# Kernel tuning notes

Measured on AMD Instinct MI355X. Metric: run time of the kernel, lower is better.

Reference implementation:

```python
import jax, jax.numpy as jnp
import numpy as np

N = 20000      # nodes
E = 320000     # edges (every node has >=1 incoming edge)
IN = 512       # input feature dim
HID = 128      # per-head hidden dim
H = 8          # heads
C = 64         # classes (final layer hidden dim)
SLOPE = 0.01   # torch F.leaky_relu default negative_slope


def _gat_head(x, src, dst, W, b, al, alb, ar, arb):
    # x: [N, D_in]; W: [D_in, D_h]; al/ar: [D_h]; alb/arb: scalar
    ft = x @ W + b                       # [N, D_h]
    a1 = ft @ al + alb                   # [N] dst-side logit
    a2 = ft @ ar + arb                   # [N] src-side logit
    s = jax.nn.leaky_relu(a1[dst] + a2[src], SLOPE)   # [E]
    smax = jax.ops.segment_max(s, dst, num_segments=N)
    e = jnp.exp(s - smax[dst])
    denom = jax.ops.segment_sum(e, dst, num_segments=N)
    w = e / denom[dst]                   # segment softmax over incoming edges
    accum = jax.ops.segment_sum(w[:, None] * ft[src], dst, num_segments=N)
    return jax.nn.elu(accum)             # GATFinalize (no residual)


def setup_inputs() -> dict:
    key = jax.random.key(0)
    ks = jax.random.split(key, 16)

    def lin(k, i, o):
        return (jax.random.normal(k, (i, o), jnp.float32) / np.sqrt(i))

    features = jax.random.normal(ks[0], (N, IN), jnp.float32)
    src = jax.random.randint(ks[1], (E,), 0, N, jnp.int32)
    dst = jnp.concatenate([
        jnp.arange(N, dtype=jnp.int32),
        jax.random.randint(ks[2], (E - N,), 0, N, jnp.int32),
    ])

    # layer 0: H heads, in_dim -> HID
    W0 = jax.random.normal(ks[3], (H, IN, HID), jnp.float32) / np.sqrt(IN)
    b0 = jnp.zeros((H, HID), jnp.float32)
    al0 = jax.random.normal(ks[4], (H, HID), jnp.float32) / np.sqrt(HID)
    alb0 = jnp.zeros((H,), jnp.float32)
    ar0 = jax.random.normal(ks[5], (H, HID), jnp.float32) / np.sqrt(HID)
    arb0 = jnp.zeros((H,), jnp.float32)

    # layer 1: H heads, H*HID -> HID
    W1 = jax.random.normal(ks[6], (H, H * HID, HID), jnp.float32) / np.sqrt(H * HID)
    b1 = jnp.zeros((H, HID), jnp.float32)
    al1 = jax.random.normal(ks[7], (H, HID), jnp.float32) / np.sqrt(HID)
    alb1 = jnp.zeros((H,), jnp.float32)
    ar1 = jax.random.normal(ks[8], (H, HID), jnp.float32) / np.sqrt(HID)
    arb1 = jnp.zeros((H,), jnp.float32)

    # final: single head, H*HID -> C
    Wf = lin(ks[9], H * HID, C)
    bf = jnp.zeros((C,), jnp.float32)
    alf = jax.random.normal(ks[10], (C,), jnp.float32) / np.sqrt(C)
    albf = jnp.zeros((), jnp.float32)
    arf = jax.random.normal(ks[11], (C,), jnp.float32) / np.sqrt(C)
    arbf = jnp.zeros((), jnp.float32)

    return dict(features=features, src=src, dst=dst,
                W0=W0, b0=b0, al0=al0, alb0=alb0, ar0=ar0, arb0=arb0,
                W1=W1, b1=b1, al1=al1, alb1=alb1, ar1=ar1, arb1=arb1,
                Wf=Wf, bf=bf, alf=alf, albf=albf, arf=arf, arbf=arbf)


def reference(features, src, dst,
              W0, b0, al0, alb0, ar0, arb0,
              W1, b1, al1, alb1, ar1, arb1,
              Wf, bf, alf, albf, arf, arbf):
    x = features
    # layer 0: concat heads -> [N, H*HID]
    x = jnp.concatenate([
        _gat_head(x, src, dst, W0[h], b0[h], al0[h], alb0[h], ar0[h], arb0[h])
        for h in range(H)], axis=1)
    # layer 1
    x = jnp.concatenate([
        _gat_head(x, src, dst, W1[h], b1[h], al1[h], alb1[h], ar1[h], arb1[h])
        for h in range(H)], axis=1)
    # final single-head output layer -> [N, C]
    return _gat_head(x, src, dst, Wf, bf, alf, albf, arf, arbf)
```

## Files before the change

kernel.cpp:

```cpp
#include <hip/hip_runtime.h>
#include <math.h>

#define N_NODES 20000
#define N_EDGES 320000
#define D_IN    512
#define D_HID   128
#define N_HEADS 8
#define N_CLS   64

typedef __bf16 bf16x8 __attribute__((ext_vector_type(8)));
typedef float  f32x4  __attribute__((ext_vector_type(4)));

__device__ __forceinline__ float leaky(float x) { return fmaxf(x, 0.01f * x); }

__device__ __forceinline__ unsigned short f2bf(float f) {
    unsigned u = __float_as_uint(f);
    return (unsigned short)((u + 0x7FFFu + ((u >> 16) & 1u)) >> 16);
}
__device__ __forceinline__ float bflo(unsigned v) { return __uint_as_float(v << 16); }
__device__ __forceinline__ float bfhi(unsigned v) { return __uint_as_float(v & 0xffff0000u); }

__device__ __forceinline__ void gl_lds16(const void* g, void* l) {
    __builtin_amdgcn_global_load_lds((const __attribute__((address_space(1))) void*)g,
                                     (__attribute__((address_space(3))) void*)l, 16, 0, 0);
}

__global__ void k_zero(int* __restrict__ p, int n) {
    int i = blockIdx.x * blockDim.x + threadIdx.x;
    if (i < n) p[i] = 0;
}

__global__ void k_count(const int* __restrict__ dst, int* __restrict__ counts, int e) {
    int i = blockIdx.x * blockDim.x + threadIdx.x;
    if (i < e) atomicAdd(&counts[dst[i]], 1);
}

__global__ void k_scan(const int* __restrict__ counts, int* __restrict__ indptr,
                       int* __restrict__ cursor, int n) {
    __shared__ int sdata[1024];
    __shared__ int srun;
    int t = threadIdx.x;
    if (t == 0) srun = 0;
    __syncthreads();
    for (int base = 0; base < n; base += 1024) {
        int idx = base + t;
        int v = (idx < n) ? counts[idx] : 0;
        sdata[t] = v;
        __syncthreads();
        for (int off = 1; off < 1024; off <<= 1) {
            int x = (t >= off) ? sdata[t - off] : 0;
            __syncthreads();
            sdata[t] += x;
            __syncthreads();
        }
        int incl = sdata[t];
        int run = srun;
        if (idx < n) {
            indptr[idx] = run + incl - v;
            cursor[idx] = run + incl - v;
        }
        __syncthreads();
        if (t == 1023) srun = run + incl;
        __syncthreads();
    }
    if (t == 0) indptr[n] = srun;
}

__global__ void k_scatter(const int* __restrict__ src, const int* __restrict__ dst,
                          int* __restrict__ cursor, int* __restrict__ csr_src, int e) {
    int i = blockIdx.x * blockDim.x + threadIdx.x;
    if (i < e) {
        int pos = atomicAdd(&cursor[dst[i]], 1);
        csr_src[pos] = src[i];
    }
}

__global__ void k_cvtA(const float* __restrict__ in, unsigned short* __restrict__ out, int n4) {
    int i = blockIdx.x * blockDim.x + threadIdx.x;
    if (i < n4) {
        float4 v = ((const float4*)in)[i];
        unsigned long long pk =
            (unsigned long long)f2bf(v.x) | ((unsigned long long)f2bf(v.y) << 16) |
            ((unsigned long long)f2bf(v.z) << 32) | ((unsigned long long)f2bf(v.w) << 48);
        *(unsigned long long*)(out + (size_t)i * 4) = pk;
    }
}

__global__ void k_cvtW(const float* __restrict__ W, unsigned short* __restrict__ Wt,
                       int K, int Nf) {
    __shared__ float t[64][65];
    int k0 = blockIdx.x * 64, n0 = blockIdx.y * 64, h = blockIdx.z;
    const float* Wh = W + (size_t)h * K * Nf;
    unsigned short* Wth = Wt + (size_t)h * K * Nf;
    int tx = threadIdx.x & 63, ty = threadIdx.x >> 6;
#pragma unroll
    for (int i = 0; i < 16; ++i) {
        int k = ty + i * 4;
        t[k][tx] = Wh[(size_t)(k0 + k) * Nf + n0 + tx];
    }
    __syncthreads();
#pragma unroll
    for (int i = 0; i < 16; ++i) {
        int n = ty + i * 4;
        Wth[(size_t)(n0 + n) * K + k0 + tx] = f2bf(t[tx][n]);
    }
}

__global__ __launch_bounds__(256) void k_gemm_fused(
    const unsigned short* __restrict__ A, const unsigned short* __restrict__ Bt,
    const float* __restrict__ bias, const float* __restrict__ al,
    const float* __restrict__ alb, const float* __restrict__ ar,
    const float* __restrict__ arb, unsigned short* __restrict__ C,
    float* __restrict__ a1, float* __restrict__ a2, int M, int K)
{
    constexpr int BM = 128, BK = 64, BNP = 256;
    __shared__ unsigned short As[BM * BK];
    __shared__ unsigned short Bs[BNP * BK];

    const int tid  = threadIdx.x;
    const int lane = tid & 63;
    const int wid  = tid >> 6;
    const int wm   = wid >> 1;
    const int wn   = wid & 1;
    const int m0   = blockIdx.x * BM;
    const int h0   = blockIdx.z * 2;
    const int h    = h0 + wn;

    const unsigned short* Bth = Bt + (size_t)h0 * 128 * K;
    const int rsub = lane & 15;
    const int rhi  = lane >> 4;
    const int wbase = tid & ~63;

    f32x4 acc[4][8];
#pragma unroll
    for (int i = 0; i < 4; ++i)
#pragma unroll
        for (int j = 0; j < 8; ++j) acc[i][j] = (f32x4){0.f, 0.f, 0.f, 0.f};

    for (int k0 = 0; k0 < K; k0 += BK) {
#pragma unroll
        for (int p = 0; p < 4; ++p) {
            int o    = (p * 256 + tid) * 16;
            int row  = o >> 7;
            int icol = (o & 127) ^ ((row & 7) << 4);
            int grow = m0 + row; if (grow > M - 1) grow = M - 1;
            gl_lds16(A + (size_t)grow * K + k0 + (icol >> 1),
                     (void*)((char*)As + (p * 256 + wbase) * 16));
        }
#pragma unroll
        for (int p = 0; p < 8; ++p) {
            int o    = (p * 256 + tid) * 16;
            int row  = o >> 7;
            int icol = (o & 127) ^ ((row & 7) << 4);
            gl_lds16(Bth + (size_t)row * K + k0 + (icol >> 1),
                     (void*)((char*)Bs + (p * 256 + wbase) * 16));
        }
        __syncthreads();

#pragma unroll
        for (int q = 0; q < 2; ++q) {
            bf16x8 av[4], bv[8];
#pragma unroll
            for (int mi = 0; mi < 4; ++mi) {
                int row  = wm * 64 + mi * 16 + rsub;
                int icol = (q * 64 + rhi * 16) ^ ((row & 7) << 4);
                av[mi] = *(const bf16x8*)((const char*)As + row * 128 + icol);
            }
#pragma unroll
            for (int ni = 0; ni < 8; ++ni) {
                int row  = wn * 128 + ni * 16 + rsub;
                int icol = (q * 64 + rhi * 16) ^ ((row & 7) << 4);
                bv[ni] = *(const bf16x8*)((const char*)Bs + row * 128 + icol);
            }
#pragma unroll
            for (int mi = 0; mi < 4; ++mi)
#pragma unroll
                for (int ni = 0; ni < 8; ++ni)
                    acc[mi][ni] = __builtin_amdgcn_mfma_f32_16x16x32_bf16(
                        av[mi], bv[ni], acc[mi][ni], 0, 0, 0);
        }
        __syncthreads();
    }

#pragma unroll
    for (int ni = 0; ni < 8; ++ni) {
        float bvv = bias[h * 128 + ni * 16 + rsub];
#pragma unroll
        for (int mi = 0; mi < 4; ++mi)
#pragma unroll
            for (int r = 0; r < 4; ++r) acc[mi][ni][r] += bvv;
    }

#pragma unroll
    for (int ni = 0; ni < 8; ++ni) {
        int col = h * 128 + ni * 16 + rsub;
#pragma unroll
        for (int mi = 0; mi < 4; ++mi) {
            int rowb = m0 + wm * 64 + mi * 16 + rhi * 4;
#pragma unroll
            for (int r = 0; r < 4; ++r) {
                int row = rowb + r;
                if (row < M) C[(size_t)row * 1024 + col] = f2bf(acc[mi][ni][r]);
            }
        }
    }

    float alv[8], arv[8];
#pragma unroll
    for (int ni = 0; ni < 8; ++ni) {
        alv[ni] = al[h * 128 + ni * 16 + rsub];
        arv[ni] = ar[h * 128 + ni * 16 + rsub];
    }
    float albv = alb[h], arbv = arb[h];
#pragma unroll
    for (int mi = 0; mi < 4; ++mi) {
#pragma unroll
        for (int r = 0; r < 4; ++r) {
            float s1 = 0.f, s2 = 0.f;
#pragma unroll
            for (int ni = 0; ni < 8; ++ni) {
                s1 += acc[mi][ni][r] * alv[ni];
                s2 += acc[mi][ni][r] * arv[ni];
            }
#pragma unroll
            for (int off = 1; off <= 8; off <<= 1) {
                s1 += __shfl_xor(s1, off);
                s2 += __shfl_xor(s2, off);
            }
            if (rsub == 0) {
                int row = m0 + wm * 64 + mi * 16 + rhi * 4 + r;
                if (row < M) {
                    a1[row * 8 + h] = s1 + albv;
                    a2[row * 8 + h] = s2 + arbv;
                }
            }
        }
    }
}

template<int BN>
__global__ __launch_bounds__(256) void k_gemm_bf16(
    const unsigned short* __restrict__ A, const unsigned short* __restrict__ Bt,
    const float* __restrict__ bias, unsigned short* __restrict__ C,
    int M, int K, int ldc)
{
    constexpr int BM = 128, BK = 64;
    constexpr int WN    = 1;
    constexpr int MFRAG = 2;
    constexpr int NFRAG = 4;

    __shared__ unsigned short As[BM * BK];
    __shared__ unsigned short Bs[BN * BK];

    const int tid  = threadIdx.x;
    const int lane = tid & 63;
    const int wid  = tid >> 6;
    const int wm   = wid / WN;
    const int wn   = wid % WN;
    const int m0   = blockIdx.x * BM;

    const int rsub = lane & 15;
    const int rhi  = lane >> 4;
    const int wbase = tid & ~63;

    f32x4 acc[MFRAG][NFRAG];
#pragma unroll
    for (int i = 0; i < MFRAG; ++i)
#pragma unroll
        for (int j = 0; j < NFRAG; ++j) acc[i][j] = (f32x4){0.f, 0.f, 0.f, 0.f};

    for (int k0 = 0; k0 < K; k0 += BK) {
#pragma unroll
        for (int p = 0; p < 4; ++p) {
            int o    = (p * 256 + tid) * 16;
            int row  = o >> 7;
            int icol = (o & 127) ^ ((row & 7) << 4);
            int grow = m0 + row; if (grow > M - 1) grow = M - 1;
            gl_lds16(A + (size_t)grow * K + k0 + (icol >> 1),
                     (void*)((char*)As + (p * 256 + wbase) * 16));
        }
#pragma unroll
        for (int p = 0; p < BN / 32; ++p) {
            int o    = (p * 256 + tid) * 16;
            int row  = o >> 7;
            int icol = (o & 127) ^ ((row & 7) << 4);
            gl_lds16(Bt + (size_t)row * K + k0 + (icol >> 1),
                     (void*)((char*)Bs + (p * 256 + wbase) * 16));
        }
        __syncthreads();

        bf16x8 av[2][MFRAG], bv[2][NFRAG];
#pragma unroll
        for (int q = 0; q < 2; ++q) {
#pragma unroll
            for (int mi = 0; mi < MFRAG; ++mi) {
                int row  = wm * (MFRAG * 16) + mi * 16 + rsub;
                int icol = (q * 64 + rhi * 16) ^ ((row & 7) << 4);
                av[q][mi] = *(const bf16x8*)((const char*)As + row * 128 + icol);
            }
#pragma unroll
            for (int ni = 0; ni < NFRAG; ++ni) {
                int row  = wn * (NFRAG * 16) + ni * 16 + rsub;
                int icol = (q * 64 + rhi * 16) ^ ((row & 7) << 4);
                bv[q][ni] = *(const bf16x8*)((const char*)Bs + row * 128 + icol);
            }
        }
#pragma unroll
        for (int q = 0; q < 2; ++q)
#pragma unroll
            for (int mi = 0; mi < MFRAG; ++mi)
#pragma unroll
                for (int ni = 0; ni < NFRAG; ++ni)
                    acc[mi][ni] = __builtin_amdgcn_mfma_f32_16x16x32_bf16(
                        av[q][mi], bv[q][ni], acc[mi][ni], 0, 0, 0);
        __syncthreads();
    }

#pragma unroll
    for (int ni = 0; ni < NFRAG; ++ni) {
        int col  = wn * (NFRAG * 16) + ni * 16 + rsub;
        float bvv = bias[col];
#pragma unroll
        for (int mi = 0; mi < MFRAG; ++mi) {
            int rowb = m0 + wm * (MFRAG * 16) + mi * 16 + rhi * 4;
#pragma unroll
            for (int r = 0; r < 4; ++r) {
                int row = rowb + r;
                if (row < M) C[(size_t)row * ldc + col] = f2bf(acc[mi][ni][r] + bvv);
            }
        }
    }
}

__global__ __launch_bounds__(256) void k_alogit(
    const unsigned short* __restrict__ ft, const float* __restrict__ al,
    const float* __restrict__ alb, const float* __restrict__ ar,
    const float* __restrict__ arb, float* __restrict__ a1,
    float* __restrict__ a2, int H_, int Dh)
{
    int n = blockIdx.x * 4 + (threadIdx.x >> 6);
    int lane = threadIdx.x & 63;
    if (n >= N_NODES) return;
    for (int h = 0; h < H_; ++h) {
        size_t base = ((size_t)h * N_NODES + n) * Dh;
        float s1 = 0.f, s2 = 0.f;
        for (int j0 = 2 * lane; j0 < Dh; j0 += 128) {
            unsigned v = *(const unsigned*)(ft + base + j0);
            float lo = bflo(v), hi = bfhi(v);
            float2 A = *(const float2*)(al + h * Dh + j0);
            float2 R = *(const float2*)(ar + h * Dh + j0);
            s1 += lo * A.x + hi * A.y;
            s2 += lo * R.x + hi * R.y;
        }
#pragma unroll
        for (int off = 32; off > 0; off >>= 1) {
            s1 += __shfl_xor(s1, off);
            s2 += __shfl_xor(s2, off);
        }
        if (lane == 0) {
            a1[n * H_ + h] = s1 + alb[h];
            a2[n * H_ + h] = s2 + arb[h];
        }
    }
}

__global__ __launch_bounds__(256) void k_aggregate_ah(
    const unsigned short* __restrict__ ft, const float* __restrict__ a1,
    const float* __restrict__ a2, const int* __restrict__ indptr,
    const int* __restrict__ csr_src, unsigned short* __restrict__ outp)
{
    __shared__ float wtab[2][4][64][8];
    __shared__ int   stab[2][4][64];

    const int wid  = threadIdx.x >> 6;
    const int lane = threadIdx.x & 63;
    int n = blockIdx.x * 4 + wid;
    if (n >= N_NODES) return;
    int start = indptr[n], end = indptr[n + 1];
    unsigned short* op = outp + (size_t)n * 1024;

    if (end <= start) {
        uint4 z = make_uint4(0, 0, 0, 0);
        *(uint4*)(op + lane * 8) = z;
        *(uint4*)(op + 512 + lane * 8) = z;
        return;
    }

    float a1v[8];
    *(float4*)&a1v[0] = *(const float4*)(a1 + n * 8);
    *(float4*)&a1v[4] = *(const float4*)(a1 + n * 8 + 4);

    float m[8], sv0[8];
    int sidx0 = 0;
#pragma unroll
    for (int h = 0; h < 8; ++h) { m[h] = -INFINITY; sv0[h] = -INFINITY; }
    {
        int e = start + lane;
        if (e < end) {
            sidx0 = csr_src[e];
            float4 x0 = *(const float4*)(a2 + (size_t)sidx0 * 8);
            float4 x1 = *(const float4*)(a2 + (size_t)sidx0 * 8 + 4);
            sv0[0] = leaky(a1v[0] + x0.x); sv0[1] = leaky(a1v[1] + x0.y);
            sv0[2] = leaky(a1v[2] + x0.z); sv0[3] = leaky(a1v[3] + x0.w);
            sv0[4] = leaky(a1v[4] + x1.x); sv0[5] = leaky(a1v[5] + x1.y);
            sv0[6] = leaky(a1v[6] + x1.z); sv0[7] = leaky(a1v[7] + x1.w);
#pragma unroll
            for (int h = 0; h < 8; ++h) m[h] = sv0[h];
        }
        for (int e2 = start + 64 + lane; e2 < end; e2 += 64) {
            int s = csr_src[e2];
            float4 x0 = *(const float4*)(a2 + (size_t)s * 8);
            float4 x1 = *(const float4*)(a2 + (size_t)s * 8 + 4);
            m[0] = fmaxf(m[0], leaky(a1v[0] + x0.x)); m[1] = fmaxf(m[1], leaky(a1v[1] + x0.y));
            m[2] = fmaxf(m[2], leaky(a1v[2] + x0.z)); m[3] = fmaxf(m[3], leaky(a1v[3] + x0.w));
            m[4] = fmaxf(m[4], leaky(a1v[4] + x1.x)); m[5] = fmaxf(m[5], leaky(a1v[5] + x1.y));
            m[6] = fmaxf(m[6], leaky(a1v[6] + x1.z)); m[7] = fmaxf(m[7], leaky(a1v[7] + x1.w));
        }
#pragma unroll
        for (int h = 0; h < 8; ++h)
#pragma unroll
            for (int off = 32; off > 0; off >>= 1)
                m[h] = fmaxf(m[h], __shfl_xor(m[h], off));
    }

    float denom[8];
    float acc[16];
#pragma unroll
    for (int h = 0; h < 8; ++h) denom[h] = 0.f;
#pragma unroll
    for (int i = 0; i < 16; ++i) acc[i] = 0.f;

    int pb = 0;
    for (int base = start; base < end; base += 64, pb ^= 1) {
        int e = base + lane;
        int cnt = min(64, end - base);
        float w[8];
        int sidx = 0;
        if (base == start) {
            sidx = sidx0;
            if (e < end) {
#pragma unroll
                for (int h = 0; h < 8; ++h) w[h] = expf(sv0[h] - m[h]);
            } else {
#pragma unroll
                for (int h = 0; h < 8; ++h) w[h] = 0.f;
            }
        } else if (e < end) {
            sidx = csr_src[e];
            float4 x0 = *(const float4*)(a2 + (size_t)sidx * 8);
            float4 x1 = *(const float4*)(a2 + (size_t)sidx * 8 + 4);
            w[0] = expf(leaky(a1v[0] + x0.x) - m[0]); w[1] = expf(leaky(a1v[1] + x0.y) - m[1]);
            w[2] = expf(leaky(a1v[2] + x0.z) - m[2]); w[3] = expf(leaky(a1v[3] + x0.w) - m[3]);
            w[4] = expf(leaky(a1v[4] + x1.x) - m[4]); w[5] = expf(leaky(a1v[5] + x1.y) - m[5]);
            w[6] = expf(leaky(a1v[6] + x1.z) - m[6]); w[7] = expf(leaky(a1v[7] + x1.w) - m[7]);
        } else {
#pragma unroll
            for (int h = 0; h < 8; ++h) w[h] = 0.f;
        }
#pragma unroll
        for (int h = 0; h < 8; ++h) denom[h] += w[h];

        *(float4*)&wtab[pb][wid][lane][0] = *(float4*)&w[0];
        *(float4*)&wtab[pb][wid][lane][4] = *(float4*)&w[4];
        stab[pb][wid][lane] = sidx;
        asm volatile("s_waitcnt lgkmcnt(0)" ::: "memory");

        const float* wrow = &wtab[pb][wid][0][0];
        const int*   srow = &stab[pb][wid][0];
        const int myh = lane >> 4;
        for (int j = 0; j < cnt; j += 2) {
            int j1ok = (j + 1 < cnt);
            int j1 = j1ok ? j + 1 : j;
            int s0 = srow[j];
            int s1 = srow[j1];
            float w00 = wrow[j * 8 + myh];
            float w01 = wrow[j * 8 + 4 + myh];
            float w10 = j1ok ? wrow[j1 * 8 + myh] : 0.f;
            float w11 = j1ok ? wrow[j1 * 8 + 4 + myh] : 0.f;
            const unsigned short* f0 = ft + (size_t)s0 * 1024;
            const unsigned short* f1 = ft + (size_t)s1 * 1024;
            uint4 v00 = *(const uint4*)(f0 + lane * 8);
            uint4 v01 = *(const uint4*)(f0 + 512 + lane * 8);
            uint4 v10 = *(const uint4*)(f1 + lane * 8);
            uint4 v11 = *(const uint4*)(f1 + 512 + lane * 8);
            acc[0]  += w00 * bflo(v00.x); acc[1]  += w00 * bfhi(v00.x);
            acc[2]  += w00 * bflo(v00.y); acc[3]  += w00 * bfhi(v00.y);
            acc[4]  += w00 * bflo(v00.z); acc[5]  += w00 * bfhi(v00.z);
            acc[6]  += w00 * bflo(v00.w); acc[7]  += w00 * bfhi(v00.w);
            acc[8]  += w01 * bflo(v01.x); acc[9]  += w01 * bfhi(v01.x);
            acc[10] += w01 * bflo(v01.y); acc[11] += w01 * bfhi(v01.y);
            acc[12] += w01 * bflo(v01.z); acc[13] += w01 * bfhi(v01.z);
            acc[14] += w01 * bflo(v01.w); acc[15] += w01 * bfhi(v01.w);
            acc[0]  += w10 * bflo(v10.x); acc[1]  += w10 * bfhi(v10.x);
            acc[2]  += w10 * bflo(v10.y); acc[3]  += w10 * bfhi(v10.y);
            acc[4]  += w10 * bflo(v10.z); acc[5]  += w10 * bfhi(v10.z);
            acc[6]  += w10 * bflo(v10.w); acc[7]  += w10 * bfhi(v10.w);
            acc[8]  += w11 * bflo(v11.x); acc[9]  += w11 * bfhi(v11.x);
            acc[10] += w11 * bflo(v11.y); acc[11] += w11 * bfhi(v11.y);
            acc[12] += w11 * bflo(v11.z); acc[13] += w11 * bfhi(v11.z);
            acc[14] += w11 * bflo(v11.w); acc[15] += w11 * bfhi(v11.w);
        }
    }

#pragma unroll
    for (int h = 0; h < 8; ++h)
#pragma unroll
        for (int off = 32; off > 0; off >>= 1)
            denom[h] += __shfl_xor(denom[h], off);

    float t01 = (lane & 16) ? denom[1] : denom[0];
    float t23 = (lane & 16) ? denom[3] : denom[2];
    float dlo = (lane & 32) ? t23 : t01;
    float t45 = (lane & 16) ? denom[5] : denom[4];
    float t67 = (lane & 16) ? denom[7] : denom[6];
    float dhi = (lane & 32) ? t67 : t45;
    float inv0 = 1.f / dlo;
    float inv1 = 1.f / dhi;

    unsigned pk[4];
#pragma unroll
    for (int u = 0; u < 4; ++u) {
        float r0 = acc[2 * u] * inv0, r1 = acc[2 * u + 1] * inv0;
        r0 = (r0 > 0.f) ? r0 : expm1f(r0);
        r1 = (r1 > 0.f) ? r1 : expm1f(r1);
        pk[u] = (unsigned)f2bf(r0) | ((unsigned)f2bf(r1) << 16);
    }
    *(uint4*)(op + lane * 8) = make_uint4(pk[0], pk[1], pk[2], pk[3]);
#pragma unroll
    for (int u = 0; u < 4; ++u) {
        float r0 = acc[8 + 2 * u] * inv1, r1 = acc[8 + 2 * u + 1] * inv1;
        r0 = (r0 > 0.f) ? r0 : expm1f(r0);
        r1 = (r1 > 0.f) ? r1 : expm1f(r1);
        pk[u] = (unsigned)f2bf(r0) | ((unsigned)f2bf(r1) << 16);
    }
    *(uint4*)(op + 512 + lane * 8) = make_uint4(pk[0], pk[1], pk[2], pk[3]);
}

__global__ __launch_bounds__(256) void k_aggregate_final(
    const unsigned short* __restrict__ ft, const float* __restrict__ a1,
    const float* __restrict__ a2, const int* __restrict__ indptr,
    const int* __restrict__ csr_src, float* __restrict__ outp)
{
    int n = blockIdx.x * 4 + (threadIdx.x >> 6);
    int lane = threadIdx.x & 63;
    if (n >= N_NODES) return;
    size_t obase = (size_t)n * 64;
    int start = indptr[n], end = indptr[n + 1];

    if (end <= start) {
        if (lane < 32) *(float2*)(outp + obase + 2 * lane) = make_float2(0.f, 0.f);
        return;
    }
    float a1v = a1[n];

    int sidx0 = 0; float sv0 = 0.f;
    float m = -INFINITY;
    {
        int e = start + lane;
        if (e < end) {
            sidx0 = csr_src[e];
            sv0 = leaky(a1v + a2[sidx0]);
            m = sv0;
        }
        for (int e2 = start + 64 + lane; e2 < end; e2 += 64)
            m = fmaxf(m, leaky(a1v + a2[csr_src[e2]]));
#pragma unroll
        for (int off = 32; off > 0; off >>= 1) m = fmaxf(m, __shfl_xor(m, off));
    }

    float denom = 0.f, acc0 = 0.f, acc1 = 0.f;
    int half = lane >> 5, idx = lane & 31;
    for (int base = start; base < end; base += 64) {
        int e = base + lane;
        float wgt = 0.f;
        int sidx = sidx0;
        if (base == start) {
            if (e < end) wgt = expf(sv0 - m);
        } else if (e < end) {
            sidx = csr_src[e];
            wgt = expf(leaky(a1v + a2[sidx]) - m);
        }
        denom += wgt;
        int cnt = min(64, end - base);
        for (int i = 0; i < cnt; i += 4) {
            int j0 = i + half, j1 = i + 2 + half;
            int jc0 = (j0 < cnt) ? j0 : (cnt - 1);
            int jc1 = (j1 < cnt) ? j1 : (cnt - 1);
            float w0 = __shfl(wgt, jc0); int s0 = __shfl(sidx, jc0);
            float w1 = __shfl(wgt, jc1); int s1 = __shfl(sidx, jc1);
            if (j0 >= cnt) w0 = 0.f;
            if (j1 >= cnt) w1 = 0.f;
            unsigned v0 = *(const unsigned*)(ft + (size_t)s0 * 64 + 2 * idx);
            unsigned v1 = *(const unsigned*)(ft + (size_t)s1 * 64 + 2 * idx);
            acc0 += w0 * bflo(v0) + w1 * bflo(v1);
            acc1 += w0 * bfhi(v0) + w1 * bfhi(v1);
        }
    }
#pragma unroll
    for (int off = 32; off > 0; off >>= 1) denom += __shfl_xor(denom, off);
    float inv = 1.f / denom;

    acc0 += __shfl_xor(acc0, 32);
    acc1 += __shfl_xor(acc1, 32);
    float r0 = acc0 * inv, r1 = acc1 * inv;
    r0 = (r0 > 0.f) ? r0 : expm1f(r0);
    r1 = (r1 > 0.f) ? r1 : expm1f(r1);
    if (lane < 32)
        *(float2*)(outp + obase + 2 * lane) = make_float2(r0, r1);
}

extern "C" void kernel_launch(void* const* d_in, const int* in_sizes, int n_in,
                              void* d_out, int out_size, void* d_ws, size_t ws_size,
                              hipStream_t stream) {
    const float* features = (const float*)d_in[0];
    const int*   src      = (const int*)d_in[1];
    const int*   dst      = (const int*)d_in[2];
    const float* W0  = (const float*)d_in[3];
    const float* b0  = (const float*)d_in[4];
    const float* al0 = (const float*)d_in[5];
    const float* alb0= (const float*)d_in[6];
    const float* ar0 = (const float*)d_in[7];
    const float* arb0= (const float*)d_in[8];
    const float* W1  = (const float*)d_in[9];
    const float* b1  = (const float*)d_in[10];
    const float* al1 = (const float*)d_in[11];
    const float* alb1= (const float*)d_in[12];
    const float* ar1 = (const float*)d_in[13];
    const float* arb1= (const float*)d_in[14];
    const float* Wf  = (const float*)d_in[15];
    const float* bff = (const float*)d_in[16];
    const float* alf = (const float*)d_in[17];
    const float* albf= (const float*)d_in[18];
    const float* arf = (const float*)d_in[19];
    const float* arbf= (const float*)d_in[20];
    float* out = (float*)d_out;

    char* wp = (char*)d_ws;
    unsigned short* ft16  = (unsigned short*)wp;  wp += (size_t)N_NODES * 1024 * 2;
    unsigned short* xb16  = (unsigned short*)wp;  wp += (size_t)N_NODES * 1024 * 2;
    unsigned short* feat16= (unsigned short*)wp;  wp += (size_t)N_NODES * 512 * 2;
    unsigned short* w0t   = (unsigned short*)wp;  wp += (size_t)N_HEADS * D_HID * D_IN * 2;
    unsigned short* w1t   = (unsigned short*)wp;  wp += (size_t)N_HEADS * D_HID * 1024 * 2;
    unsigned short* wft   = (unsigned short*)wp;  wp += (size_t)N_CLS * 1024 * 2;
    float* a1             = (float*)wp;           wp += (size_t)N_NODES * N_HEADS * 4;
    float* a2             = (float*)wp;           wp += (size_t)N_NODES * N_HEADS * 4;
    int* counts = (int*)wp;                       wp += (size_t)N_NODES * 4;
    int* indptr = (int*)wp;                       wp += (size_t)(N_NODES + 1) * 4;
    int* cursor = (int*)wp;                       wp += (size_t)N_NODES * 4;
    int* csr    = (int*)wp;

    k_zero<<<(N_NODES + 255) / 256, 256, 0, stream>>>(counts, N_NODES);
    k_count<<<(N_EDGES + 255) / 256, 256, 0, stream>>>(dst, counts, N_EDGES);
    k_scan<<<1, 1024, 0, stream>>>(counts, indptr, cursor, N_NODES);
    k_scatter<<<(N_EDGES + 255) / 256, 256, 0, stream>>>(src, dst, cursor, csr, N_EDGES);

    k_cvtA<<<(N_NODES * D_IN / 4 + 255) / 256, 256, 0, stream>>>(features, feat16, N_NODES * D_IN / 4);
    k_cvtW<<<dim3(D_IN / 64, D_HID / 64, N_HEADS), 256, 0, stream>>>(W0, w0t, D_IN, D_HID);
    k_cvtW<<<dim3(1024 / 64, D_HID / 64, N_HEADS), 256, 0, stream>>>(W1, w1t, 1024, D_HID);
    k_cvtW<<<dim3(1024 / 64, N_CLS / 64, 1), 256, 0, stream>>>(Wf, wft, 1024, N_CLS);

    const int gm = (N_NODES + 127) / 128;
    int nodeBlocks = (N_NODES + 3) / 4;

    k_gemm_fused<<<dim3(gm, 1, N_HEADS / 2), 256, 0, stream>>>(
        feat16, w0t, b0, al0, alb0, ar0, arb0, ft16, a1, a2, N_NODES, D_IN);
    k_aggregate_ah<<<nodeBlocks, 256, 0, stream>>>(ft16, a1, a2, indptr, csr, xb16);

    k_gemm_fused<<<dim3(gm, 1, N_HEADS / 2), 256, 0, stream>>>(
        xb16, w1t, b1, al1, alb1, ar1, arb1, ft16, a1, a2, N_NODES, 1024);
    k_aggregate_ah<<<nodeBlocks, 256, 0, stream>>>(ft16, a1, a2, indptr, csr, xb16);

    k_gemm_bf16<64><<<dim3(gm, 1, 1), 256, 0, stream>>>(
        xb16, wft, bff, ft16, N_NODES, 1024, N_CLS);
    k_alogit<<<nodeBlocks, 256, 0, stream>>>(ft16, alf, albf, arf, arbf, a1, a2, 1, N_CLS);
    k_aggregate_final<<<nodeBlocks, 256, 0, stream>>>(ft16, a1, a2, indptr, csr, out);
}
```

Before: 616.7 us.

## Shrink fused GEMM tile to one head per block with transposed MFMA epilogue

The fused GEMM+attention-logit kernel now handles one head per block (BN=128 instead of two heads at 256), which halves accumulator registers and doubles the grid so more blocks are resident. The MFMA operands are swapped so each lane holds 4 consecutive output columns, allowing packed 8-byte bf16 stores and float4 loads of bias and attention vectors. Logit partial sums from the two column-warps are combined through shared memory. The cost is more reloading of the A tile across heads and an extra block-level sync.

```diff
diff --git a/kernel.cpp b/kernel.cpp
--- a/kernel.cpp
+++ b/kernel.cpp
@@ -113,9 +113,10 @@
     const float* __restrict__ arb, unsigned short* __restrict__ C,
     float* __restrict__ a1, float* __restrict__ a2, int M, int K)
 {
-    constexpr int BM = 128, BK = 64, BNP = 256;
+    constexpr int BM = 128, BK = 64, BN = 128;
     __shared__ unsigned short As[BM * BK];
-    __shared__ unsigned short Bs[BNP * BK];
+    __shared__ unsigned short Bs[BN * BK];
+    __shared__ float p1[4][64], p2[4][64];
 
     const int tid  = threadIdx.x;
     const int lane = tid & 63;
@@ -123,19 +124,18 @@
     const int wm   = wid >> 1;
     const int wn   = wid & 1;
     const int m0   = blockIdx.x * BM;
-    const int h0   = blockIdx.z * 2;
-    const int h    = h0 + wn;
-
-    const unsigned short* Bth = Bt + (size_t)h0 * 128 * K;
+    const int h    = blockIdx.z;
+
+    const unsigned short* Bth = Bt + (size_t)h * 128 * K;
     const int rsub = lane & 15;
     const int rhi  = lane >> 4;
     const int wbase = tid & ~63;
 
-    f32x4 acc[4][8];
+    f32x4 accT[4][4];
 #pragma unroll
     for (int i = 0; i < 4; ++i)
 #pragma unroll
-        for (int j = 0; j < 8; ++j) acc[i][j] = (f32x4){0.f, 0.f, 0.f, 0.f};
+        for (int j = 0; j < 4; ++j) accT[i][j] = (f32x4){0.f, 0.f, 0.f, 0.f};
 
     for (int k0 = 0; k0 < K; k0 += BK) {
 #pragma unroll
@@ -148,7 +148,7 @@
                      (void*)((char*)As + (p * 256 + wbase) * 16));
         }
 #pragma unroll
-        for (int p = 0; p < 8; ++p) {
+        for (int p = 0; p < 4; ++p) {
             int o    = (p * 256 + tid) * 16;
             int row  = o >> 7;
             int icol = (o & 127) ^ ((row & 7) << 4);
@@ -159,7 +159,7 @@
 
 #pragma unroll
         for (int q = 0; q < 2; ++q) {
-            bf16x8 av[4], bv[8];
+            bf16x8 av[4], bv[4];
 #pragma unroll
             for (int mi = 0; mi < 4; ++mi) {
                 int row  = wm * 64 + mi * 16 + rsub;
@@ -167,72 +167,78 @@
                 av[mi] = *(const bf16x8*)((const char*)As + row * 128 + icol);
             }
 #pragma unroll
-            for (int ni = 0; ni < 8; ++ni) {
-                int row  = wn * 128 + ni * 16 + rsub;
+            for (int ni = 0; ni < 4; ++ni) {
+                int row  = wn * 64 + ni * 16 + rsub;
                 int icol = (q * 64 + rhi * 16) ^ ((row & 7) << 4);
                 bv[ni] = *(const bf16x8*)((const char*)Bs + row * 128 + icol);
             }
 #pragma unroll
-            for (int mi = 0; mi < 4; ++mi)
-#pragma unroll
-                for (int ni = 0; ni < 8; ++ni)
-                    acc[mi][ni] = __builtin_amdgcn_mfma_f32_16x16x32_bf16(
-                        av[mi], bv[ni], acc[mi][ni], 0, 0, 0);
+            for (int ni = 0; ni < 4; ++ni)
+#pragma unroll
+                for (int mi = 0; mi < 4; ++mi)
+                    accT[ni][mi] = __builtin_amdgcn_mfma_f32_16x16x32_bf16(
+                        bv[ni], av[mi], accT[ni][mi], 0, 0, 0);
         }
         __syncthreads();
     }
 
-#pragma unroll
-    for (int ni = 0; ni < 8; ++ni) {
-        float bvv = bias[h * 128 + ni * 16 + rsub];
-#pragma unroll
-        for (int mi = 0; mi < 4; ++mi)
-#pragma unroll
-            for (int r = 0; r < 4; ++r) acc[mi][ni][r] += bvv;
-    }
-
-#pragma unroll
-    for (int ni = 0; ni < 8; ++ni) {
-        int col = h * 128 + ni * 16 + rsub;
+    float4 al4[4], ar4[4];
+#pragma unroll
+    for (int ni = 0; ni < 4; ++ni) {
+        int nb = wn * 64 + ni * 16 + rhi * 4;
+        float4 b4 = *(const float4*)&bias[h * 128 + nb];
+        al4[ni] = *(const float4*)&al[h * 128 + nb];
+        ar4[ni] = *(const float4*)&ar[h * 128 + nb];
 #pragma unroll
         for (int mi = 0; mi < 4; ++mi) {
-            int rowb = m0 + wm * 64 + mi * 16 + rhi * 4;
-#pragma unroll
-            for (int r = 0; r < 4; ++r) {
-                int row = rowb + r;
-                if (row < M) C[(size_t)row * 1024 + col] = f2bf(acc[mi][ni][r]);
-            }
-        }
-    }
-
-    float alv[8], arv[8];
-#pragma unroll
-    for (int ni = 0; ni < 8; ++ni) {
-        alv[ni] = al[h * 128 + ni * 16 + rsub];
-        arv[ni] = ar[h * 128 + ni * 16 + rsub];
-    }
-    float albv = alb[h], arbv = arb[h];
+            accT[ni][mi][0] += b4.x; accT[ni][mi][1] += b4.y;
+            accT[ni][mi][2] += b4.z; accT[ni][mi][3] += b4.w;
+        }
+    }
+
 #pragma unroll
     for (int mi = 0; mi < 4; ++mi) {
-#pragma unroll
-        for (int r = 0; r < 4; ++r) {
-            float s1 = 0.f, s2 = 0.f;
-#pragma unroll
-            for (int ni = 0; ni < 8; ++ni) {
-                s1 += acc[mi][ni][r] * alv[ni];
-                s2 += acc[mi][ni][r] * arv[ni];
-            }
-#pragma unroll
-            for (int off = 1; off <= 8; off <<= 1) {
-                s1 += __shfl_xor(s1, off);
-                s2 += __shfl_xor(s2, off);
-            }
-            if (rsub == 0) {
-                int row = m0 + wm * 64 + mi * 16 + rhi * 4 + r;
-                if (row < M) {
-                    a1[row * 8 + h] = s1 + albv;
-                    a2[row * 8 + h] = s2 + arbv;
-                }
+        int m = m0 + wm * 64 + mi * 16 + rsub;
+        if (m >= M) continue;
+        unsigned short* cp = C + (size_t)m * 1024 + h * 128 + wn * 64 + rhi * 4;
+#pragma unroll
+        for (int ni = 0; ni < 4; ++ni) {
+            unsigned long long pk =
+                (unsigned long long)f2bf(accT[ni][mi][0]) |
+                ((unsigned long long)f2bf(accT[ni][mi][1]) << 16) |
+                ((unsigned long long)f2bf(accT[ni][mi][2]) << 32) |
+                ((unsigned long long)f2bf(accT[ni][mi][3]) << 48);
+            *(unsigned long long*)(cp + ni * 16) = pk;
+        }
+    }
+
+#pragma unroll
+    for (int mi = 0; mi < 4; ++mi) {
+        float s1 = 0.f, s2 = 0.f;
+#pragma unroll
+        for (int ni = 0; ni < 4; ++ni) {
+            s1 += accT[ni][mi][0] * al4[ni].x + accT[ni][mi][1] * al4[ni].y
+                + accT[ni][mi][2] * al4[ni].z + accT[ni][mi][3] * al4[ni].w;
+            s2 += accT[ni][mi][0] * ar4[ni].x + accT[ni][mi][1] * ar4[ni].y
+                + accT[ni][mi][2] * ar4[ni].z + accT[ni][mi][3] * ar4[ni].w;
+        }
+        s1 += __shfl_xor(s1, 16); s1 += __shfl_xor(s1, 32);
+        s2 += __shfl_xor(s2, 16); s2 += __shfl_xor(s2, 32);
+        if (rhi == 0) {
+            p1[wid][mi * 16 + rsub] = s1;
+            p2[wid][mi * 16 + rsub] = s2;
+        }
+    }
+    __syncthreads();
+    if (wn == 0 && rhi == 0) {
+        float albv = alb[h], arbv = arb[h];
+#pragma unroll
+        for (int mi = 0; mi < 4; ++mi) {
+            int rl = mi * 16 + rsub;
+            int row = m0 + wm * 64 + rl;
+            if (row < M) {
+                a1[row * 8 + h] = p1[wm * 2][rl] + p1[wm * 2 + 1][rl] + albv;
+                a2[row * 8 + h] = p2[wm * 2][rl] + p2[wm * 2 + 1][rl] + arbv;
             }
         }
     }
@@ -662,11 +668,11 @@
     const int gm = (N_NODES + 127) / 128;
     int nodeBlocks = (N_NODES + 3) / 4;
 
-    k_gemm_fused<<<dim3(gm, 1, N_HEADS / 2), 256, 0, stream>>>(
+    k_gemm_fused<<<dim3(gm, 1, N_HEADS), 256, 0, stream>>>(
         feat16, w0t, b0, al0, alb0, ar0, arb0, ft16, a1, a2, N_NODES, D_IN);
     k_aggregate_ah<<<nodeBlocks, 256, 0, stream>>>(ft16, a1, a2, indptr, csr, xb16);
 
-    k_gemm_fused<<<dim3(gm, 1, N_HEADS / 2), 256, 0, stream>>>(
+    k_gemm_fused<<<dim3(gm, 1, N_HEADS), 256, 0, stream>>>(
         xb16, w1t, b1, al1, alb1, ar1, arb1, ft16, a1, a2, N_NODES, 1024);
     k_aggregate_ah<<<nodeBlocks, 256, 0, stream>>>(ft16, a1, a2, indptr, csr, xb16);
 
```

Result: faster. 556.8 us (-9.7%).
